# Performance work log

Measured on AMD Instinct MI355X. Metric: run time of the kernel, lower is better.

## Reference

```python
import jax, jax.numpy as jnp
import numpy as np

B, T, E, H = 4, 4096, 1024, 64

def setup_inputs() -> dict:
    key = jax.random.key(0)
    kx, kk, kq, kv = jax.random.split(key, 4)
    return {
        "x": jax.random.normal(kx, (B, T, E), dtype=jnp.float32),
        "Wk": jax.random.normal(kk, (E, H), dtype=jnp.float32) * (E ** -0.5),
        "Wq": jax.random.normal(kq, (E, H), dtype=jnp.float32) * (E ** -0.5),
        "Wv": jax.random.normal(kv, (E, H), dtype=jnp.float32) * (E ** -0.5),
    }

def reference(x, Wk, Wq, Wv):
    # x: [B, T, E]; projections: [B, T, H]
    k = jnp.einsum("bte,eh->bth", x, Wk)
    q = jnp.einsum("bte,eh->bth", x, Wq)
    v = jnp.einsum("bte,eh->bth", x, Wv)
    # NOTE: original scales by embedding dim (x.shape[-1]), not head dim.
    scale = x.shape[-1] ** -0.5
    scores = jnp.einsum("bqh,bkh->bqk", q, k) * scale  # [B, T, T]
    t = x.shape[1]
    causal = jnp.tril(jnp.ones((t, t), dtype=bool))
    scores = jnp.where(causal[None, :, :], scores, -jnp.inf)
    attn = jax.nn.softmax(scores, axis=-1)
    # dropout_rate = 0 (eval) -> identity
    return jnp.einsum("bqk,bkh->bqh", attn, v)
```

## Files before the change

### kernel.cpp

```cpp
#include <hip/hip_runtime.h>
#include <hip/hip_bf16.h>

typedef __attribute__((ext_vector_type(8))) short s16x8;
typedef __attribute__((ext_vector_type(4))) float f32x4;

#define TSEQ 4096
#define SPLIT 8

static __device__ __forceinline__ ushort f2bf(float f) {
    union { float f; unsigned u; } v; v.f = f;
    unsigned u = v.u;
    unsigned r = (u + 0x7fffu + ((u >> 16) & 1u)) >> 16;
    return (ushort)r;
}

static __device__ __forceinline__ float bf2f(unsigned lo16) {
    union { unsigned u; float f; } v; v.u = lo16 << 16; return v.f;
}

static __device__ __forceinline__ float fexp2(float x) {
    float r; asm("v_exp_f32 %0, %1" : "=v"(r) : "v"(x)); return r;
}

static __device__ __forceinline__ s16x8 mk8(unsigned a, unsigned b, unsigned c, unsigned d) {
    union { uint4 u; s16x8 v; } x; x.u = make_uint4(a, b, c, d); return x.v;
}

static __device__ __forceinline__ void gload_lds16(const void* g, void* l) {
    __builtin_amdgcn_global_load_lds(
        (const __attribute__((address_space(1))) unsigned int*)g,
        (__attribute__((address_space(3))) unsigned int*)l, 16, 0, 0);
}

__global__ __launch_bounds__(256) void prep_w(const float* __restrict__ Wk,
                                              const float* __restrict__ Wq,
                                              const float* __restrict__ Wv,
                                              ushort* __restrict__ wt) {
    __shared__ float tile[64][65];
    int bid = blockIdx.x;
    int mi = bid >> 4;
    int e0 = (bid & 15) << 6;
    const float* src = (mi == 0) ? Wq : (mi == 1) ? Wk : Wv;
    int n = threadIdx.x & 63;
    int quad = threadIdx.x >> 6;
#pragma unroll
    for (int r = 0; r < 16; ++r) {
        int el = r * 4 + quad;
        tile[el][n] = src[(size_t)(e0 + el) * 64 + n];
    }
    __syncthreads();
    float scale = (mi == 0) ? 0.045084224f : 1.0f;
    int ecol = threadIdx.x & 63;
#pragma unroll
    for (int r = 0; r < 16; ++r) {
        int nl = r * 4 + quad;
        wt[(size_t)(mi * 64 + nl) * 1024 + e0 + ecol] = f2bf(tile[ecol][nl] * scale);
    }
}

__global__ __launch_bounds__(512) void proj(const float* __restrict__ x,
                                            const ushort* __restrict__ wt,
                                            ushort* __restrict__ qb,
                                            ushort* __restrict__ kb,
                                            ushort* __restrict__ vt) {
    __shared__ char smem[3 * 40960];
    int tid = threadIdx.x;
    int lane = tid & 63, w = tid >> 6;
    int l15 = lane & 15, g = lane >> 4;
    int mh = w >> 2, nq = w & 3;
    size_t m0 = (size_t)blockIdx.x * 64;

    int rA = tid >> 4, sA = tid & 15;
    const float* xsrc = x + (m0 + rA) * 1024 + ((sA ^ (rA & 15)) << 2);
    int rB = tid >> 3, sB = tid & 7;
    const ushort* wsrc = wt + (size_t)rB * 1024 + ((sB ^ (rB & 7)) << 3);

    f32x4 acc[2][3];
#pragma unroll
    for (int mi = 0; mi < 2; ++mi)
#pragma unroll
        for (int j = 0; j < 3; ++j) acc[mi][j] = (f32x4){0.f, 0.f, 0.f, 0.f};

#define PSTAGE(bufsel, it) do {                                        \
        size_t k0_ = (size_t)(it) << 6;                                \
        char* bb_ = smem + (bufsel) * 40960;                           \
        gload_lds16(xsrc + k0_, bb_ + tid * 16);                       \
        gload_lds16(xsrc + 32 * 1024 + k0_, bb_ + 8192 + tid * 16);    \
        gload_lds16(wsrc + k0_, bb_ + 16384 + tid * 16);               \
        gload_lds16(wsrc + 64 * 1024 + k0_, bb_ + 24576 + tid * 16);   \
        gload_lds16(wsrc + 128 * 1024 + k0_, bb_ + 32768 + tid * 16);  \
    } while (0)

    PSTAGE(0, 0);
    PSTAGE(1, 1);
    for (int i = 0; i < 16; ++i) {
        int cur = i % 3;
        __builtin_amdgcn_sched_barrier(0);
        if (i < 15) asm volatile("s_waitcnt vmcnt(5)" ::: "memory");
        else        asm volatile("s_waitcnt vmcnt(0)" ::: "memory");
        __builtin_amdgcn_s_barrier();
        __builtin_amdgcn_sched_barrier(0);
        if (i + 2 < 16) PSTAGE((i + 2) % 3, i + 2);

        const char* Ab = smem + cur * 40960;
        const char* Bb = Ab + 16384;
#pragma unroll
        for (int ks = 0; ks < 2; ++ks) {
            s16x8 a[2];
#pragma unroll
            for (int mi = 0; mi < 2; ++mi) {
                int row = mh * 32 + mi * 16 + l15;
                int s0 = ks * 8 + g * 2;
                f32x4 xa = *(const f32x4*)(Ab + row * 256 + ((s0 ^ l15) << 4));
                f32x4 xb2 = *(const f32x4*)(Ab + row * 256 + (((s0 + 1) ^ l15) << 4));
#pragma unroll
                for (int q2 = 0; q2 < 4; ++q2) {
                    a[mi][q2] = (short)f2bf(xa[q2]);
                    a[mi][q2 + 4] = (short)f2bf(xb2[q2]);
                }
            }
#pragma unroll
            for (int j = 0; j < 3; ++j) {
                int n = nq * 48 + j * 16 + l15;
                s16x8 bf = *(const s16x8*)(Bb + n * 128 + (((ks * 4 + g) ^ (l15 & 7)) << 4));
#pragma unroll
                for (int mi = 0; mi < 2; ++mi)
                    acc[mi][j] = __builtin_amdgcn_mfma_f32_16x16x32_bf16(a[mi], bf, acc[mi][j], 0, 0, 0);
            }
        }
    }
#undef PSTAGE

    size_t bb = m0 >> 12;
    size_t t00 = m0 & 4095;
#pragma unroll
    for (int mi = 0; mi < 2; ++mi) {
        size_t Mb = m0 + mh * 32 + mi * 16 + 4 * g;
#pragma unroll
        for (int j = 0; j < 3; ++j) {
            int nf = nq * 3 + j;
            int n = nf * 16 + l15;
            if (nf < 4) {
#pragma unroll
                for (int r = 0; r < 4; ++r)
                    qb[(Mb + r) * 64 + n] = f2bf(acc[mi][j][r]);
            } else if (nf < 8) {
#pragma unroll
                for (int r = 0; r < 4; ++r)
                    kb[(Mb + r) * 64 + (n - 64)] = f2bf(acc[mi][j][r]);
            } else {
                int h = n - 128;
                size_t tloc = t00 + mh * 32 + mi * 16 + 4 * g;
                unsigned w0 = (unsigned)f2bf(acc[mi][j][0]) | ((unsigned)f2bf(acc[mi][j][1]) << 16);
                unsigned w1 = (unsigned)f2bf(acc[mi][j][2]) | ((unsigned)f2bf(acc[mi][j][3]) << 16);
                *(uint2*)(vt + (bb * 64 + h) * TSEQ + tloc) = make_uint2(w0, w1);
            }
        }
    }
}

__global__ __launch_bounds__(512) void attn(const ushort* __restrict__ qb,
                                            const ushort* __restrict__ kb,
                                            const ushort* __restrict__ vt,
                                            ushort* __restrict__ po,
                                            float2* __restrict__ pml) {
    __shared__ char smem[49152];
    int tid = threadIdx.x;
    int lane = tid & 63, w = tid >> 6;
    int l15 = lane & 15, g = lane >> 4;
    int bid = blockIdx.x;
    int s = bid & 7;
    int b = (bid >> 3) & 3;
    int idx = bid >> 5;
    int p = (idx < 16) ? (31 - idx) : (idx - 16);
    int q0w = p * 128 + w * 16;
    int q = q0w + l15;
    int my_tmax = q0w >> 6;
    int nkvb = 2 * p + 2;
    int cnt = (s < nkvb) ? ((nkvb + 7 - s) >> 3) : 0;

    int row = tid >> 3;
    int kswz = (((tid & 7) ^ (row & 7)) << 3);

    const ushort* qbase = qb + ((size_t)b * TSEQ + q) * 64;
    s16x8 qf0 = *(const s16x8*)(qbase + g * 8);
    s16x8 qf1 = *(const s16x8*)(qbase + 32 + g * 8);

    f32x4 o[4];
#pragma unroll
    for (int i = 0; i < 4; ++i) o[i] = (f32x4){0.f, 0.f, 0.f, 0.f};
    float m = -1e30f, lsum = 0.f;

#define STAGE(bufsel, tt) do {                                                         \
        const ushort* ksrc_ = kb + ((size_t)b * TSEQ + (size_t)(tt) * 64 + row) * 64 + kswz; \
        gload_lds16(ksrc_, smem + (bufsel) * 8192 + tid * 16);                         \
        const ushort* vsrc_ = vt + ((size_t)b * 64 + row) * TSEQ + (size_t)(tt) * 64 + kswz; \
        gload_lds16(vsrc_, smem + 24576 + (bufsel) * 8192 + tid * 16);                 \
    } while (0)

    if (cnt > 0) {
        STAGE(0, s);
        if (cnt > 1) STAGE(1, s + 8);
        for (int i = 0; i < cnt; ++i) {
            int t = s + (i << 3);
            int cur = i % 3;
            __builtin_amdgcn_sched_barrier(0);
            if (i + 1 < cnt) asm volatile("s_waitcnt vmcnt(2)" ::: "memory");
            else             asm volatile("s_waitcnt vmcnt(0)" ::: "memory");
            __builtin_amdgcn_s_barrier();
            __builtin_amdgcn_sched_barrier(0);
            if (i + 2 < cnt) STAGE((i + 2) % 3, t + 16);

            if (t <= my_tmax) {
                const char* Kb = smem + cur * 8192;
                const char* Vb = smem + 24576 + cur * 8192;
                int swz = (l15 & 7) << 4;

                f32x4 st[4];
#pragma unroll
                for (int kf = 0; kf < 4; ++kf) {
                    const char* kr = Kb + (kf * 16 + l15) * 128;
                    s16x8 ka0 = *(const s16x8*)(kr + ((g * 16) ^ swz));
                    s16x8 ka1 = *(const s16x8*)(kr + ((64 + g * 16) ^ swz));
                    f32x4 z = (f32x4){0.f, 0.f, 0.f, 0.f};
                    z = __builtin_amdgcn_mfma_f32_16x16x32_bf16(ka0, qf0, z, 0, 0, 0);
                    st[kf] = __builtin_amdgcn_mfma_f32_16x16x32_bf16(ka1, qf1, z, 0, 0, 0);
                }

                if (t == my_tmax) {
#pragma unroll
                    for (int kf = 0; kf < 4; ++kf) {
#pragma unroll
                        for (int r = 0; r < 4; ++r) {
                            int k = (t << 6) + kf * 16 + 4 * g + r;
                            if (k > q) st[kf][r] = -1e30f;
                        }
                    }
                }

                float pmax = st[0][0];
#pragma unroll
                for (int kf = 0; kf < 4; ++kf) {
#pragma unroll
                    for (int r = 0; r < 4; ++r) pmax = fmaxf(pmax, st[kf][r]);
                }
                pmax = fmaxf(pmax, __shfl_xor(pmax, 16, 64));
                pmax = fmaxf(pmax, __shfl_xor(pmax, 32, 64));

                if (!__all(pmax - m <= 8.0f)) {
                    float mnew = fmaxf(m, pmax);
                    float sf = fexp2(m - mnew);
                    m = mnew;
                    lsum *= sf;
#pragma unroll
                    for (int i2 = 0; i2 < 4; ++i2) {
                        o[i2][0] *= sf; o[i2][1] *= sf; o[i2][2] *= sf; o[i2][3] *= sf;
                    }
                }

                float psum = 0.f;
                ushort pb[4][4];
#pragma unroll
                for (int kf = 0; kf < 4; ++kf) {
#pragma unroll
                    for (int r = 0; r < 4; ++r) {
                        float pv = fexp2(st[kf][r] - m);
                        psum += pv;
                        pb[kf][r] = f2bf(pv);
                    }
                }
                lsum += psum;

                unsigned pw[4][2];
#pragma unroll
                for (int kf = 0; kf < 4; ++kf) {
                    pw[kf][0] = (unsigned)pb[kf][0] | ((unsigned)pb[kf][1] << 16);
                    pw[kf][1] = (unsigned)pb[kf][2] | ((unsigned)pb[kf][3] << 16);
                }
#pragma unroll
                for (int ks = 0; ks < 2; ++ks) {
                    s16x8 pf = mk8(pw[2 * ks][0], pw[2 * ks][1], pw[2 * ks + 1][0], pw[2 * ks + 1][1]);
#pragma unroll
                    for (int hf = 0; hf < 4; ++hf) {
                        const char* vr = Vb + (hf * 16 + l15) * 128;
                        uint2 lo = *(const uint2*)(vr + ((ks * 64 + g * 8) ^ swz));
                        uint2 hi = *(const uint2*)(vr + ((ks * 64 + 32 + g * 8) ^ swz));
                        o[hf] = __builtin_amdgcn_mfma_f32_16x16x32_bf16(
                            mk8(lo.x, lo.y, hi.x, hi.y), pf, o[hf], 0, 0, 0);
                    }
                }
            }
        }
    }
#undef STAGE

    __syncthreads();

    lsum += __shfl_xor(lsum, 16, 64);
    lsum += __shfl_xor(lsum, 32, 64);

    float* ot = (float*)(smem + w * 4352);
#pragma unroll
    for (int hf = 0; hf < 4; ++hf) {
#pragma unroll
        for (int r = 0; r < 4; ++r)
            ot[l15 * 68 + hf * 16 + 4 * g + r] = o[hf][r];
    }
    int rowq = lane >> 2, quad = lane & 3;
    const float* src = &ot[rowq * 68 + quad * 16];
    unsigned pk[8];
#pragma unroll
    for (int j = 0; j < 8; ++j)
        pk[j] = (unsigned)f2bf(src[2 * j]) | ((unsigned)f2bf(src[2 * j + 1]) << 16);
    ushort* dst = po + ((size_t)s * 16384 + b * 4096 + q0w + rowq) * 64 + quad * 16;
    *(uint4*)dst = make_uint4(pk[0], pk[1], pk[2], pk[3]);
    *(uint4*)(dst + 8) = make_uint4(pk[4], pk[5], pk[6], pk[7]);

    if (lane < 16) {
        pml[(size_t)s * 16384 + b * 4096 + q0w + l15] = make_float2(m, lsum);
    }
}

__global__ __launch_bounds__(256) void merge(const ushort* __restrict__ po,
                                             const float2* __restrict__ pml,
                                             float* __restrict__ out) {
    int gt = blockIdx.x * 256 + threadIdx.x;
    int rowq = gt >> 4;
    int h4 = (gt & 15) << 2;
    float ms[SPLIT], ls[SPLIT];
    float M = -1e30f;
#pragma unroll
    for (int s2 = 0; s2 < SPLIT; ++s2) {
        float2 ml = pml[(size_t)s2 * 16384 + rowq];
        ms[s2] = ml.x; ls[s2] = ml.y;
        M = fmaxf(M, ml.x);
    }
    float L = 0.f;
    float ww[SPLIT];
#pragma unroll
    for (int s2 = 0; s2 < SPLIT; ++s2) {
        float e = fexp2(ms[s2] - M);
        ww[s2] = e;
        L += ls[s2] * e;
    }
    f32x4 acc = (f32x4){0.f, 0.f, 0.f, 0.f};
#pragma unroll
    for (int s2 = 0; s2 < SPLIT; ++s2) {
        uint2 pv = *(const uint2*)(po + ((size_t)s2 * 16384 + rowq) * 64 + h4);
        float wgt = ww[s2];
        acc[0] += wgt * bf2f(pv.x & 0xffffu);
        acc[1] += wgt * bf2f(pv.x >> 16);
        acc[2] += wgt * bf2f(pv.y & 0xffffu);
        acc[3] += wgt * bf2f(pv.y >> 16);
    }
    float inv = 1.0f / L;
    *(f32x4*)(out + (size_t)rowq * 64 + h4) = acc * inv;
}

extern "C" void kernel_launch(void* const* d_in, const int* in_sizes, int n_in,
                              void* d_out, int out_size, void* d_ws, size_t ws_size,
                              hipStream_t stream) {
    (void)in_sizes; (void)n_in; (void)out_size; (void)ws_size;
    const float* x  = (const float*)d_in[0];
    const float* Wk = (const float*)d_in[1];
    const float* Wq = (const float*)d_in[2];
    const float* Wv = (const float*)d_in[3];
    float* out = (float*)d_out;

    char* ws = (char*)d_ws;
    ushort* wt = (ushort*)(ws);
    ushort* qb = (ushort*)(ws + (1u << 20));
    ushort* kb = (ushort*)(ws + (3u << 20));
    ushort* vt = (ushort*)(ws + (5u << 20));
    ushort* po = (ushort*)(ws + ((size_t)8 << 20));
    float2* pml = (float2*)(ws + ((size_t)26 << 20));

    prep_w<<<48, 256, 0, stream>>>(Wk, Wq, Wv, wt);
    proj<<<256, 512, 0, stream>>>(x, wt, qb, kb, vt);
    attn<<<1024, 512, 0, stream>>>(qb, kb, vt, po, pml);
    merge<<<1024, 256, 0, stream>>>(po, pml, out);
}
```

Before: 139.4 us.

## Use 128-wide KV tiles with double buffering and halve split-K count

The attention kernel now processes 128-key tiles per iteration instead of 64, uses two LDS buffers (64 KB) instead of three, and splits the KV range 4 ways instead of 8, which halves the grid. Each tile now does twice the MFMA work per barrier, so there are fewer synchronisations and less per-tile overhead, and the merge step has fewer partial results to combine. The trade-offs are larger register and LDS use, a second barrier per iteration so the next tile can be prefetched into the buffer just consumed, and fewer blocks in flight for the causal workload, which can hurt load balance.

```diff
diff --git a/kernel.cpp b/kernel.cpp
--- a/kernel.cpp
+++ b/kernel.cpp
@@ -5,7 +5,7 @@
 typedef __attribute__((ext_vector_type(4))) float f32x4;
 
 #define TSEQ 4096
-#define SPLIT 8
+#define SPLIT 4
 
 static __device__ __forceinline__ ushort f2bf(float f) {
     union { float f; unsigned u; } v; v.f = f;
@@ -159,30 +159,32 @@
     }
 }
 
-__global__ __launch_bounds__(512) void attn(const ushort* __restrict__ qb,
-                                            const ushort* __restrict__ kb,
-                                            const ushort* __restrict__ vt,
-                                            ushort* __restrict__ po,
-                                            float2* __restrict__ pml) {
-    __shared__ char smem[49152];
+__global__ __launch_bounds__(512, 2) void attn(const ushort* __restrict__ qb,
+                                               const ushort* __restrict__ kb,
+                                               const ushort* __restrict__ vt,
+                                               ushort* __restrict__ po,
+                                               float2* __restrict__ pml) {
+    __shared__ char smem[65536];
+    char* smK = smem;
+    char* smV = smem + 32768;
     int tid = threadIdx.x;
     int lane = tid & 63, w = tid >> 6;
     int l15 = lane & 15, g = lane >> 4;
     int bid = blockIdx.x;
-    int s = bid & 7;
-    int b = (bid >> 3) & 3;
-    int idx = bid >> 5;
+    int s = bid & 3;
+    int b = (bid >> 2) & 3;
+    int idx = bid >> 4;
     int p = (idx < 16) ? (31 - idx) : (idx - 16);
     int q0w = p * 128 + w * 16;
-    int q = q0w + l15;
-    int my_tmax = q0w >> 6;
-    int nkvb = 2 * p + 2;
-    int cnt = (s < nkvb) ? ((nkvb + 7 - s) >> 3) : 0;
-
-    int row = tid >> 3;
-    int kswz = (((tid & 7) ^ (row & 7)) << 3);
-
-    const ushort* qbase = qb + ((size_t)b * TSEQ + q) * 64;
+    int nkvt = p + 1;
+    int cnt = (s < nkvt) ? ((nkvt - s + 3) >> 2) : 0;
+
+    int rK = tid >> 3;
+    int kxs = (((tid & 7) ^ (rK & 7)) << 3);
+    int hV = tid >> 4;
+    int vxs = (((tid & 15) ^ (hV & 15)) << 3);
+
+    const ushort* qbase = qb + ((size_t)b * TSEQ + q0w + l15) * 64;
     s16x8 qf0 = *(const s16x8*)(qbase + g * 8);
     s16x8 qf1 = *(const s16x8*)(qbase + 32 + g * 8);
 
@@ -191,105 +193,105 @@
     for (int i = 0; i < 4; ++i) o[i] = (f32x4){0.f, 0.f, 0.f, 0.f};
     float m = -1e30f, lsum = 0.f;
 
-#define STAGE(bufsel, tt) do {                                                         \
-        const ushort* ksrc_ = kb + ((size_t)b * TSEQ + (size_t)(tt) * 64 + row) * 64 + kswz; \
-        gload_lds16(ksrc_, smem + (bufsel) * 8192 + tid * 16);                         \
-        const ushort* vsrc_ = vt + ((size_t)b * 64 + row) * TSEQ + (size_t)(tt) * 64 + kswz; \
-        gload_lds16(vsrc_, smem + 24576 + (bufsel) * 8192 + tid * 16);                 \
+#define STAGE(bufsel, tt) do {                                                          \
+        const ushort* kA_ = kb + ((size_t)b * TSEQ + (size_t)(tt) * 128 + rK) * 64 + kxs; \
+        gload_lds16(kA_, smK + (bufsel) * 16384 + tid * 16);                            \
+        gload_lds16(kA_ + 64 * 64, smK + (bufsel) * 16384 + 8192 + tid * 16);           \
+        const ushort* vA_ = vt + ((size_t)b * 64 + hV) * TSEQ + (size_t)(tt) * 128 + vxs; \
+        gload_lds16(vA_, smV + (bufsel) * 16384 + tid * 16);                            \
+        gload_lds16(vA_ + 32 * TSEQ, smV + (bufsel) * 16384 + 8192 + tid * 16);         \
     } while (0)
 
     if (cnt > 0) {
         STAGE(0, s);
-        if (cnt > 1) STAGE(1, s + 8);
+        if (cnt > 1) STAGE(1, s + 4);
         for (int i = 0; i < cnt; ++i) {
-            int t = s + (i << 3);
-            int cur = i % 3;
+            int t = s + (i << 2);
+            int cur = i & 1;
             __builtin_amdgcn_sched_barrier(0);
-            if (i + 1 < cnt) asm volatile("s_waitcnt vmcnt(2)" ::: "memory");
+            if (i + 1 < cnt) asm volatile("s_waitcnt vmcnt(4)" ::: "memory");
             else             asm volatile("s_waitcnt vmcnt(0)" ::: "memory");
             __builtin_amdgcn_s_barrier();
             __builtin_amdgcn_sched_barrier(0);
-            if (i + 2 < cnt) STAGE((i + 2) % 3, t + 16);
-
-            if (t <= my_tmax) {
-                const char* Kb = smem + cur * 8192;
-                const char* Vb = smem + 24576 + cur * 8192;
-                int swz = (l15 & 7) << 4;
-
-                f32x4 st[4];
-#pragma unroll
-                for (int kf = 0; kf < 4; ++kf) {
-                    const char* kr = Kb + (kf * 16 + l15) * 128;
-                    s16x8 ka0 = *(const s16x8*)(kr + ((g * 16) ^ swz));
-                    s16x8 ka1 = *(const s16x8*)(kr + ((64 + g * 16) ^ swz));
-                    f32x4 z = (f32x4){0.f, 0.f, 0.f, 0.f};
-                    z = __builtin_amdgcn_mfma_f32_16x16x32_bf16(ka0, qf0, z, 0, 0, 0);
-                    st[kf] = __builtin_amdgcn_mfma_f32_16x16x32_bf16(ka1, qf1, z, 0, 0, 0);
-                }
-
-                if (t == my_tmax) {
-#pragma unroll
-                    for (int kf = 0; kf < 4; ++kf) {
-#pragma unroll
-                        for (int r = 0; r < 4; ++r) {
-                            int k = (t << 6) + kf * 16 + 4 * g + r;
-                            if (k > q) st[kf][r] = -1e30f;
-                        }
+
+            const char* Kb = smK + cur * 16384;
+            const char* Vb = smV + cur * 16384;
+            int swzk = (l15 & 7) << 4;
+
+            f32x4 st[8];
+#pragma unroll
+            for (int kf = 0; kf < 8; ++kf) {
+                const char* kr = Kb + (kf * 16 + l15) * 128;
+                s16x8 ka0 = *(const s16x8*)(kr + ((g << 4) ^ swzk));
+                s16x8 ka1 = *(const s16x8*)(kr + (((4 + g) << 4) ^ swzk));
+                f32x4 z = (f32x4){0.f, 0.f, 0.f, 0.f};
+                z = __builtin_amdgcn_mfma_f32_16x16x32_bf16(ka0, qf0, z, 0, 0, 0);
+                st[kf] = __builtin_amdgcn_mfma_f32_16x16x32_bf16(ka1, qf1, z, 0, 0, 0);
+            }
+
+            if (t == p) {
+                int ql = w * 16 + l15;
+#pragma unroll
+                for (int kf = 0; kf < 8; ++kf) {
+#pragma unroll
+                    for (int r = 0; r < 4; ++r) {
+                        if (kf * 16 + 4 * g + r > ql) st[kf][r] = -1e30f;
                     }
                 }
-
-                float pmax = st[0][0];
-#pragma unroll
-                for (int kf = 0; kf < 4; ++kf) {
-#pragma unroll
-                    for (int r = 0; r < 4; ++r) pmax = fmaxf(pmax, st[kf][r]);
+            }
+
+            float pmax = st[0][0];
+#pragma unroll
+            for (int kf = 0; kf < 8; ++kf) {
+#pragma unroll
+                for (int r = 0; r < 4; ++r) pmax = fmaxf(pmax, st[kf][r]);
+            }
+            pmax = fmaxf(pmax, __shfl_xor(pmax, 16, 64));
+            pmax = fmaxf(pmax, __shfl_xor(pmax, 32, 64));
+
+            if (!__all(pmax - m <= 8.0f)) {
+                float mnew = fmaxf(m, pmax);
+                float sf = fexp2(m - mnew);
+                m = mnew;
+                lsum *= sf;
+#pragma unroll
+                for (int i2 = 0; i2 < 4; ++i2) {
+                    o[i2][0] *= sf; o[i2][1] *= sf; o[i2][2] *= sf; o[i2][3] *= sf;
                 }
-                pmax = fmaxf(pmax, __shfl_xor(pmax, 16, 64));
-                pmax = fmaxf(pmax, __shfl_xor(pmax, 32, 64));
-
-                if (!__all(pmax - m <= 8.0f)) {
-                    float mnew = fmaxf(m, pmax);
-                    float sf = fexp2(m - mnew);
-                    m = mnew;
-                    lsum *= sf;
-#pragma unroll
-                    for (int i2 = 0; i2 < 4; ++i2) {
-                        o[i2][0] *= sf; o[i2][1] *= sf; o[i2][2] *= sf; o[i2][3] *= sf;
-                    }
+            }
+
+            float psum = 0.f;
+            unsigned pw[8][2];
+#pragma unroll
+            for (int kf = 0; kf < 8; ++kf) {
+                float p0 = fexp2(st[kf][0] - m);
+                float p1 = fexp2(st[kf][1] - m);
+                float p2 = fexp2(st[kf][2] - m);
+                float p3 = fexp2(st[kf][3] - m);
+                psum += (p0 + p1) + (p2 + p3);
+                pw[kf][0] = (unsigned)f2bf(p0) | ((unsigned)f2bf(p1) << 16);
+                pw[kf][1] = (unsigned)f2bf(p2) | ((unsigned)f2bf(p3) << 16);
+            }
+            lsum += psum;
+
+#pragma unroll
+            for (int ks = 0; ks < 4; ++ks) {
+                s16x8 pf = mk8(pw[2 * ks][0], pw[2 * ks][1], pw[2 * ks + 1][0], pw[2 * ks + 1][1]);
+#pragma unroll
+                for (int hf = 0; hf < 4; ++hf) {
+                    const char* vr = Vb + (hf * 16 + l15) * 256;
+                    int j0 = ks * 4 + (g >> 1), o0 = (g & 1) * 8;
+                    uint2 lo = *(const uint2*)(vr + ((j0 ^ l15) << 4) + o0);
+                    uint2 hi = *(const uint2*)(vr + (((j0 + 2) ^ l15) << 4) + o0);
+                    o[hf] = __builtin_amdgcn_mfma_f32_16x16x32_bf16(
+                        mk8(lo.x, lo.y, hi.x, hi.y), pf, o[hf], 0, 0, 0);
                 }
-
-                float psum = 0.f;
-                ushort pb[4][4];
-#pragma unroll
-                for (int kf = 0; kf < 4; ++kf) {
-#pragma unroll
-                    for (int r = 0; r < 4; ++r) {
-                        float pv = fexp2(st[kf][r] - m);
-                        psum += pv;
-                        pb[kf][r] = f2bf(pv);
-                    }
-                }
-                lsum += psum;
-
-                unsigned pw[4][2];
-#pragma unroll
-                for (int kf = 0; kf < 4; ++kf) {
-                    pw[kf][0] = (unsigned)pb[kf][0] | ((unsigned)pb[kf][1] << 16);
-                    pw[kf][1] = (unsigned)pb[kf][2] | ((unsigned)pb[kf][3] << 16);
-                }
-#pragma unroll
-                for (int ks = 0; ks < 2; ++ks) {
-                    s16x8 pf = mk8(pw[2 * ks][0], pw[2 * ks][1], pw[2 * ks + 1][0], pw[2 * ks + 1][1]);
-#pragma unroll
-                    for (int hf = 0; hf < 4; ++hf) {
-                        const char* vr = Vb + (hf * 16 + l15) * 128;
-                        uint2 lo = *(const uint2*)(vr + ((ks * 64 + g * 8) ^ swz));
-                        uint2 hi = *(const uint2*)(vr + ((ks * 64 + 32 + g * 8) ^ swz));
-                        o[hf] = __builtin_amdgcn_mfma_f32_16x16x32_bf16(
-                            mk8(lo.x, lo.y, hi.x, hi.y), pf, o[hf], 0, 0, 0);
-                    }
-                }
-            }
+            }
+
+            __builtin_amdgcn_sched_barrier(0);
+            __builtin_amdgcn_s_barrier();
+            __builtin_amdgcn_sched_barrier(0);
+            if (i + 2 < cnt) STAGE(cur, t + 8);
         }
     }
 #undef STAGE
@@ -307,11 +309,11 @@
             ot[l15 * 68 + hf * 16 + 4 * g + r] = o[hf][r];
     }
     int rowq = lane >> 2, quad = lane & 3;
-    const float* src = &ot[rowq * 68 + quad * 16];
+    const float* srcp = &ot[rowq * 68 + quad * 16];
     unsigned pk[8];
 #pragma unroll
     for (int j = 0; j < 8; ++j)
-        pk[j] = (unsigned)f2bf(src[2 * j]) | ((unsigned)f2bf(src[2 * j + 1]) << 16);
+        pk[j] = (unsigned)f2bf(srcp[2 * j]) | ((unsigned)f2bf(srcp[2 * j + 1]) << 16);
     ushort* dst = po + ((size_t)s * 16384 + b * 4096 + q0w + rowq) * 64 + quad * 16;
     *(uint4*)dst = make_uint4(pk[0], pk[1], pk[2], pk[3]);
     *(uint4*)(dst + 8) = make_uint4(pk[4], pk[5], pk[6], pk[7]);
@@ -373,10 +375,10 @@
     ushort* kb = (ushort*)(ws + (3u << 20));
     ushort* vt = (ushort*)(ws + (5u << 20));
     ushort* po = (ushort*)(ws + ((size_t)8 << 20));
-    float2* pml = (float2*)(ws + ((size_t)26 << 20));
+    float2* pml = (float2*)(ws + ((size_t)17 << 20));
 
     prep_w<<<48, 256, 0, stream>>>(Wk, Wq, Wv, wt);
     proj<<<256, 512, 0, stream>>>(x, wt, qb, kb, vt);
-    attn<<<1024, 512, 0, stream>>>(qb, kb, vt, po, pml);
+    attn<<<512, 512, 0, stream>>>(qb, kb, vt, po, pml);
     merge<<<1024, 256, 0, stream>>>(po, pml, out);
 }
```

Result: faster. 134.6 us (-3.4%).
